# Kernel optimization log

Measured on AMD Instinct MI355X. Metric: run time of the kernel, lower is better.

The kernel has to match this reference:

```python
import jax, jax.numpy as jnp
import numpy as np

EPS = 1e-4   # synsin-style z clamp in world_to_view
BIG = 1e10   # z-buffer init


def _xy_grid(h, w):
    xs = jnp.linspace(-1.0, 1.0, w)
    ys = jnp.linspace(-1.0, 1.0, h)
    gy, gx = jnp.meshgrid(ys, xs, indexing='ij')
    return jnp.stack([gx.ravel(), gy.ravel()], 0)  # [2, h*w], NDC pixel rays


def _view_to_world(depth, K_inv, RTinv, xy):
    # depth [B,1,N]; homogeneous coords rows = (x*d, y*d, d, 1)
    proj = jnp.concatenate([xy[None] * depth, depth, jnp.ones_like(depth)], axis=1)  # [B,4,N]
    cam = jnp.einsum('bij,bjn->bin', K_inv, proj)
    return jnp.einsum('bij,bjn->bin', RTinv, cam)  # [B,4,N]


def _world_to_view(world, K, RT):
    cam2 = jnp.einsum('bij,bjn->bin', RT, world)
    xy_proj = jnp.einsum('bij,bjn->bin', K, cam2)
    z = xy_proj[:, 2:3]
    mask = jnp.abs(z) < EPS
    zs = jnp.where(mask, EPS, z)
    sampler = jnp.concatenate([xy_proj[:, 0:2] / zs, z], axis=1)  # [B,3,N]
    return jnp.where(mask, -10.0, sampler)


def _splat_one(sampler, feats, h, w):
    # sampler [3,N] (x,y in NDC, z depth); feats [C,N]. Nearest-pixel z-buffer splat.
    x, y, z = sampler[0], sampler[1], sampler[2]
    n = x.shape[0]
    px = jnp.round((x + 1.0) * 0.5 * (w - 1)).astype(jnp.int32)
    py = jnp.round((y + 1.0) * 0.5 * (h - 1)).astype(jnp.int32)
    valid = (px >= 0) & (px < w) & (py >= 0) & (py < h) & (z > EPS)
    idx = jnp.where(valid, py * w + px, h * w)  # invalid -> dump bucket h*w
    zv = jnp.where(valid, z, BIG)
    zbuf = jnp.full(h * w + 1, BIG, feats.dtype).at[idx].min(zv)
    pid = jnp.where(valid & (zv <= zbuf[idx]), jnp.arange(n, dtype=jnp.int32), n)
    win = jnp.full(h * w + 1, n, jnp.int32).at[idx].min(pid)[: h * w]  # winning point per pixel
    fpad = jnp.concatenate([feats, jnp.zeros((feats.shape[0], 1), feats.dtype)], axis=1)
    out = fpad[:, win].reshape(feats.shape[0], h, w)
    zb = zbuf[: h * w]
    depth = jnp.where(zb < BIG, zb, 0.0).reshape(1, h, w)
    return out, depth


def _project(depths, colors, feats, K, src_RTs, src_RTinvs, dst_RTs, dst_RTinvs):
    B, V, _, Hc, Wc = depths.shape
    _, _, C, Hf, Wf = feats.shape
    sh, sw = Hf / Hc, Wf / Wc
    scale = jnp.array([sw, sh, 1.0, 1.0], depths.dtype)[None, :, None]
    sK = K * scale
    sKinv = jnp.linalg.inv(sK)

    colors_r = jax.image.resize(colors.reshape(B * V, 3, Hc, Wc), (B * V, 3, Hf, Wf),
                                method='linear', antialias=True)
    depths_r = jax.image.resize(depths.reshape(B * V, 1, Hc, Wc), (B * V, 1, Hf, Wf),
                                method='nearest')
    feats_f = feats.reshape(B, V, C, Hf * Wf)
    colors_f = colors_r.reshape(B, V, 3, Hf * Wf)
    depths_f = depths_r.reshape(B, V, 1, Hf * Wf)

    xy = _xy_grid(Hf, Wf)
    dstRT = dst_RTs[:, 0]  # num_outputs == 1
    splat = jax.vmap(lambda s, f: _splat_one(s, f, Hf, Wf))

    results, warped, pdepths = [], [], []
    for i in range(V):  # small fixed number of source views
        world = _view_to_world(depths_f[:, i], sKinv, src_RTinvs[:, i], xy)
        sampler = _world_to_view(world, sK, dstRT)            # [B,3,N]
        src = jnp.concatenate([feats_f[:, i], colors_f[:, i] * 0.5 + 0.5], axis=1)  # [B,C+3,N]
        res, dep = splat(sampler, src)                        # [B,C+3,Hf,Wf], [B,1,Hf,Wf]
        results.append(res[:, :C])
        warped.append(res[:, C:])
        pdepths.append(dep)

    prj_fs = jnp.stack(results, 0)      # [V,B,C,Hf,Wf]
    warped = jnp.stack(warped, 0)       # [V,B,3,Hf,Wf]
    prj_depths = jnp.stack(pdepths, 0)  # [V,B,1,Hf,Wf]
    # forward() permutes prj_fs / prj_depths to [B,V,...]; warped stays [V,B,...]
    return prj_fs.transpose(1, 0, 2, 3, 4), warped, prj_depths.transpose(1, 0, 2, 3, 4)


def setup_inputs() -> dict:
    key = jax.random.key(0)
    k1, k2, k3 = jax.random.split(key, 3)
    B, V, Hc, Wc = 2, 2, 512, 512
    Hf, Wf, C = 256, 256, 64

    depths = jax.random.uniform(k1, (B, V, 1, Hc, Wc), jnp.float32, 1.0, 5.0)
    colors = jax.random.uniform(k2, (B, V, 3, Hc, Wc), jnp.float32, -1.0, 1.0)
    feats = jax.random.normal(k3, (B, V, C, Hf, Wf), jnp.float32)

    K = np.eye(4, dtype=np.float32)  # NDC intrinsic (fx=fy=1, cx=cy=0)
    th = 0.1
    R = np.array([[np.cos(th), 0, np.sin(th), 0.2],
                  [0, 1, 0, 0.0],
                  [-np.sin(th), 0, np.cos(th), 0.1],
                  [0, 0, 0, 1]], dtype=np.float32)
    src_RT = np.eye(4, dtype=np.float32)

    Kb = jnp.asarray(np.tile(K[None], (B, 1, 1)))
    src_RTs = jnp.asarray(np.tile(src_RT[None, None], (B, V, 1, 1)))
    src_RTinvs = src_RTs  # identity
    dst_RTs = jnp.asarray(np.tile(R[None, None], (B, 1, 1, 1)))
    dst_RTinvs = jnp.asarray(np.tile(np.linalg.inv(R)[None, None], (B, 1, 1, 1)))

    return {"depths": depths, "colors": colors, "feats": feats, "K": Kb,
            "src_RTs": src_RTs, "src_RTinvs": src_RTinvs,
            "dst_RTs": dst_RTs, "dst_RTinvs": dst_RTinvs}


def reference(depths, colors, feats, K, src_RTs, src_RTinvs, dst_RTs, dst_RTinvs):
    return _project(depths, colors, feats, K, src_RTs, src_RTinvs, dst_RTs, dst_RTinvs)
```

## Files before the change

### kernel.cpp

```cpp
#include <hip/hip_runtime.h>
#include <stdint.h>

#pragma clang fp contract(off)

namespace {
constexpr int B_ = 2, V_ = 2, HC = 512, WC = 512, HF = 256, WF = 256, CF = 64;
constexpr int NPIX = HF * WF;
constexpr float EPSF = 1e-4f;
constexpr float BIGF = 1e10f;
constexpr int NPT = B_ * V_ * NPIX;
constexpr int NBLK_PT = NPT / 256;
constexpr int RESIZE_BLKS = (B_ * V_ * 3 * NPIX) / 256;
constexpr int TP_BLKS = B_ * V_ * (NPIX / 64);
constexpr size_t WS_BASE = (size_t)NPT * 8 + (size_t)B_ * V_ * 3 * NPIX * 4 + 256;
constexpr size_t TF_BYTES = (size_t)NPT * CF * 4;
}

__device__ __forceinline__ float dot4f(const float* __restrict__ r,
                                       float v0, float v1, float v2, float v3) {
  float t = r[0] * v0;
  t = t + r[1] * v1;
  t = t + r[2] * v2;
  t = t + r[3] * v3;
  return t;
}

__global__ void init_k(const float* __restrict__ K,
                       float* __restrict__ mats,
                       unsigned long long* __restrict__ zwin) {
  int g = blockIdx.x * blockDim.x + threadIdx.x;
  zwin[g] = ~0ULL;

  if (g < B_) {
    int b = g;
    const float rowscale[4] = {0.5f, 0.5f, 1.0f, 1.0f};
    float sK[16];
    for (int i = 0; i < 4; ++i)
      for (int j = 0; j < 4; ++j)
        sK[i*4+j] = K[b*16 + i*4 + j] * rowscale[i];
    double m[16];
    for (int i = 0; i < 16; ++i) m[i] = (double)sK[i];
    double inv[16];
    inv[0]  =  m[5]*m[10]*m[15] - m[5]*m[11]*m[14] - m[9]*m[6]*m[15] + m[9]*m[7]*m[14] + m[13]*m[6]*m[11] - m[13]*m[7]*m[10];
    inv[4]  = -m[4]*m[10]*m[15] + m[4]*m[11]*m[14] + m[8]*m[6]*m[15] - m[8]*m[7]*m[14] - m[12]*m[6]*m[11] + m[12]*m[7]*m[10];
    inv[8]  =  m[4]*m[9]*m[15]  - m[4]*m[11]*m[13] - m[8]*m[5]*m[15] + m[8]*m[7]*m[13] + m[12]*m[5]*m[11] - m[12]*m[7]*m[9];
    inv[12] = -m[4]*m[9]*m[14]  + m[4]*m[10]*m[13] + m[8]*m[5]*m[14] - m[8]*m[6]*m[13] - m[12]*m[5]*m[10] + m[12]*m[6]*m[9];
    inv[1]  = -m[1]*m[10]*m[15] + m[1]*m[11]*m[14] + m[9]*m[2]*m[15] - m[9]*m[3]*m[14] - m[13]*m[2]*m[11] + m[13]*m[3]*m[10];
    inv[5]  =  m[0]*m[10]*m[15] - m[0]*m[11]*m[14] - m[8]*m[2]*m[15] + m[8]*m[3]*m[14] + m[12]*m[2]*m[11] - m[12]*m[3]*m[10];
    inv[9]  = -m[0]*m[9]*m[15]  + m[0]*m[11]*m[13] + m[8]*m[1]*m[15] - m[8]*m[3]*m[13] - m[12]*m[1]*m[11] + m[12]*m[3]*m[9];
    inv[13] =  m[0]*m[9]*m[14]  - m[0]*m[10]*m[13] - m[8]*m[1]*m[14] + m[8]*m[2]*m[13] + m[12]*m[1]*m[10] - m[12]*m[2]*m[9];
    inv[2]  =  m[1]*m[6]*m[15]  - m[1]*m[7]*m[14]  - m[5]*m[2]*m[15] + m[5]*m[3]*m[14] + m[13]*m[2]*m[7]  - m[13]*m[3]*m[6];
    inv[6]  = -m[0]*m[6]*m[15]  + m[0]*m[7]*m[14]  + m[4]*m[2]*m[15] - m[4]*m[3]*m[14] - m[12]*m[2]*m[7]  + m[12]*m[3]*m[6];
    inv[10] =  m[0]*m[5]*m[15]  - m[0]*m[7]*m[13]  - m[4]*m[1]*m[15] + m[4]*m[3]*m[13] + m[12]*m[1]*m[7]  - m[12]*m[3]*m[5];
    inv[14] = -m[0]*m[5]*m[14]  + m[0]*m[6]*m[13]  + m[4]*m[1]*m[14] - m[4]*m[2]*m[13] - m[12]*m[1]*m[6]  + m[12]*m[2]*m[5];
    inv[3]  = -m[1]*m[6]*m[11]  + m[1]*m[7]*m[10]  + m[5]*m[2]*m[11] - m[5]*m[3]*m[10] - m[9]*m[2]*m[7]   + m[9]*m[3]*m[6];
    inv[7]  =  m[0]*m[6]*m[11]  - m[0]*m[7]*m[10]  - m[4]*m[2]*m[11] + m[4]*m[3]*m[10] + m[8]*m[2]*m[7]   - m[8]*m[3]*m[6];
    inv[11] = -m[0]*m[5]*m[11]  + m[0]*m[7]*m[9]   + m[4]*m[1]*m[11] - m[4]*m[3]*m[9]  - m[8]*m[1]*m[7]   + m[8]*m[3]*m[5];
    inv[15] =  m[0]*m[5]*m[10]  - m[0]*m[6]*m[9]   - m[4]*m[1]*m[10] + m[4]*m[2]*m[9]  + m[8]*m[1]*m[6]   - m[8]*m[2]*m[5];
    double det = m[0]*inv[0] + m[1]*inv[4] + m[2]*inv[8] + m[3]*inv[12];
    double idet = 1.0 / det;
    for (int i = 0; i < 16; ++i) {
      mats[b*32 + i]      = sK[i];
      mats[b*32 + 16 + i] = (float)(inv[i] * idet);
    }
  }
}

__global__ void work_k(const float* __restrict__ depths,
                       const float* __restrict__ mats,
                       const float* __restrict__ srcRTinv,
                       const float* __restrict__ dstRT,
                       unsigned long long* __restrict__ zwin,
                       const float* __restrict__ feats,
                       float* __restrict__ tf,
                       const float* __restrict__ colors,
                       float* __restrict__ colr) {
  int bid = blockIdx.x;
  int nTP = (int)gridDim.x - RESIZE_BLKS - NBLK_PT;
  int t = threadIdx.x;

  if (bid < nTP) {
    int bv = bid >> 10;
    int pix0 = (bid & 1023) << 6;
    int c4 = t >> 4;
    int p4 = t & 15;
    const float* fb = feats + (size_t)bv * CF * NPIX + pix0 + 4 * p4;
    float4 v0 = *(const float4*)(fb + (size_t)(4 * c4 + 0) * NPIX);
    float4 v1 = *(const float4*)(fb + (size_t)(4 * c4 + 1) * NPIX);
    float4 v2 = *(const float4*)(fb + (size_t)(4 * c4 + 2) * NPIX);
    float4 v3 = *(const float4*)(fb + (size_t)(4 * c4 + 3) * NPIX);
    float* tb = tf + ((size_t)bv * NPIX + pix0 + 4 * p4) * CF + 4 * c4;
    *(float4*)(tb + 0 * CF) = make_float4(v0.x, v1.x, v2.x, v3.x);
    *(float4*)(tb + 1 * CF) = make_float4(v0.y, v1.y, v2.y, v3.y);
    *(float4*)(tb + 2 * CF) = make_float4(v0.z, v1.z, v2.z, v3.z);
    *(float4*)(tb + 3 * CF) = make_float4(v0.w, v1.w, v2.w, v3.w);
    return;
  }

  int rb = bid - nTP;
  if (rb < RESIZE_BLKS) {
    int g = rb * 256 + t;
    int pc  = g >> 16;
    int pix = g & (NPIX - 1);
    int y = pix >> 8, x = pix & (WF - 1);
    const float* src = colors + (size_t)pc * HC * WC;
    const float W37 = (float)(3.0 / 7.0), W17 = (float)(1.0 / 7.0);
    float wy[4] = {0.125f, 0.375f, 0.375f, 0.125f};
    float wx[4] = {0.125f, 0.375f, 0.375f, 0.125f};
    if (y == 0)      { wy[0] = 0.f; wy[1] = W37; wy[2] = W37; wy[3] = W17; }
    if (y == HF - 1) { wy[0] = W17; wy[1] = W37; wy[2] = W37; wy[3] = 0.f; }
    if (x == 0)      { wx[0] = 0.f; wx[1] = W37; wx[2] = W37; wx[3] = W17; }
    if (x == WF - 1) { wx[0] = W17; wx[1] = W37; wx[2] = W37; wx[3] = 0.f; }
    int jy0 = 2 * y - 1, jx0 = 2 * x - 1;
    float acc = 0.f;
    #pragma unroll
    for (int ty = 0; ty < 4; ++ty) {
      if (wy[ty] == 0.f) continue;
      int jy = jy0 + ty;
      float rs = 0.f;
      #pragma unroll
      for (int tx = 0; tx < 4; ++tx) {
        if (wx[tx] == 0.f) continue;
        rs = rs + wx[tx] * src[(size_t)jy * WC + (jx0 + tx)];
      }
      acc = acc + wy[ty] * rs;
    }
    colr[g] = acc;
    return;
  }

  int g = (rb - RESIZE_BLKS) * 256 + t;
  if (g >= NPT) return;
  int bv = g >> 16;
  int n  = g & (NPIX - 1);
  int b  = bv / V_;
  int y = n >> 8, x = n & (WF - 1);
  float d = depths[(size_t)bv * HC * WC + (size_t)(2 * y + 1) * WC + (2 * x + 1)];
  const float step32 = 2.0f / 255.0f;
  float xf = (float)x * step32 - 1.0f;
  float yf = (float)y * step32 - 1.0f;
  float pr0 = xf * d, pr1 = yf * d, pr2 = d, pr3 = 1.0f;
  const float* sK  = mats + b * 32;
  const float* sKi = mats + b * 32 + 16;
  const float* Rs  = srcRTinv + (size_t)bv * 16;
  const float* Rd  = dstRT + (size_t)b * 16;
  float a0 = dot4f(sKi + 0,  pr0, pr1, pr2, pr3);
  float a1 = dot4f(sKi + 4,  pr0, pr1, pr2, pr3);
  float a2 = dot4f(sKi + 8,  pr0, pr1, pr2, pr3);
  float a3 = dot4f(sKi + 12, pr0, pr1, pr2, pr3);
  float w0 = dot4f(Rs + 0,  a0, a1, a2, a3);
  float w1 = dot4f(Rs + 4,  a0, a1, a2, a3);
  float w2 = dot4f(Rs + 8,  a0, a1, a2, a3);
  float w3 = dot4f(Rs + 12, a0, a1, a2, a3);
  float c0 = dot4f(Rd + 0,  w0, w1, w2, w3);
  float c1 = dot4f(Rd + 4,  w0, w1, w2, w3);
  float c2 = dot4f(Rd + 8,  w0, w1, w2, w3);
  float c3 = dot4f(Rd + 12, w0, w1, w2, w3);
  float p0 = dot4f(sK + 0, c0, c1, c2, c3);
  float p1 = dot4f(sK + 4, c0, c1, c2, c3);
  float p2 = dot4f(sK + 8, c0, c1, c2, c3);
  if (!(p2 > EPSF)) return;
  float sx = p0 / p2, sy = p1 / p2;
  float pxf = rintf(((sx + 1.0f) * 0.5f) * 255.0f);
  float pyf = rintf(((sy + 1.0f) * 0.5f) * 255.0f);
  if (!(pxf >= 0.0f && pxf <= 255.0f && pyf >= 0.0f && pyf <= 255.0f)) return;
  int idx = (int)pyf * WF + (int)pxf;
  unsigned zbits = __float_as_uint(p2);
  unsigned long long key = ((unsigned long long)zbits << 32) | (unsigned)n;
  atomicMin(&zwin[(size_t)bv * NPIX + idx], key);
}

__global__ void gather3_k(const unsigned long long* __restrict__ zwin,
                          const float* __restrict__ tf,
                          const float* __restrict__ colr,
                          float* __restrict__ out0,
                          float* __restrict__ out1,
                          float* __restrict__ out2) {
  int bid = blockIdx.x;
  int grp = bid >> 10;
  int g   = (bid & (NBLK_PT - 1)) * 256 + threadIdx.x;
  int bv  = g >> 16;
  int pix = g & (NPIX - 1);
  unsigned long long key = zwin[g];
  bool hit = (key != ~0ULL);
  int n = (int)(key & 0xffffffffULL);

  if (grp < 2) {
    float4 f[8];
    if (hit) {
      const float4* src =
          (const float4*)(tf + ((size_t)bv * NPIX + n) * CF + grp * 32);
      #pragma unroll
      for (int i = 0; i < 8; ++i) f[i] = src[i];
    } else {
      #pragma unroll
      for (int i = 0; i < 8; ++i) f[i] = make_float4(0.f, 0.f, 0.f, 0.f);
    }
    float* o0 = out0 + (size_t)bv * CF * NPIX + (size_t)(grp * 32) * NPIX + pix;
    const float* fs = (const float*)f;
    #pragma unroll
    for (int c = 0; c < 32; ++c)
      __builtin_nontemporal_store(fs[c], &o0[(size_t)c * NPIX]);
  } else {
    int b = bv >> 1, v = bv & 1;
    const float* cb = colr + (size_t)bv * 3 * NPIX;
    float* o1 = out1 + (size_t)(v * B_ + b) * 3 * NPIX + pix;
    if (hit) {
      float z = __uint_as_float((unsigned)(key >> 32));
      __builtin_nontemporal_store((z < BIGF) ? z : 0.0f, &out2[g]);
      #pragma unroll
      for (int ch = 0; ch < 3; ++ch)
        __builtin_nontemporal_store(cb[(size_t)ch * NPIX + n] * 0.5f + 0.5f,
                                    &o1[(size_t)ch * NPIX]);
    } else {
      __builtin_nontemporal_store(0.0f, &out2[g]);
      #pragma unroll
      for (int ch = 0; ch < 3; ++ch)
        __builtin_nontemporal_store(0.0f, &o1[(size_t)ch * NPIX]);
    }
  }
}

__global__ void gather_k(const unsigned long long* __restrict__ zwin,
                         const float* __restrict__ feats,
                         const float* __restrict__ colr,
                         float* __restrict__ out0,
                         float* __restrict__ out1,
                         float* __restrict__ out2) {
  int bid = blockIdx.x;
  int grp = bid >> 10;
  int g   = (bid & (NBLK_PT - 1)) * 256 + threadIdx.x;
  int bv  = g >> 16;
  int pix = g & (NPIX - 1);
  unsigned long long key = zwin[g];
  bool hit = (key != ~0ULL);
  int n = (int)(key & 0xffffffffULL);

  if (grp < 4) {
    int c0 = grp * 16;
    const float* fb = feats + (size_t)bv * CF * NPIX + (size_t)c0 * NPIX;
    float* o0 = out0 + (size_t)bv * CF * NPIX + (size_t)c0 * NPIX + pix;
    if (hit) {
      #pragma unroll
      for (int c = 0; c < 16; ++c)
        __builtin_nontemporal_store(fb[(size_t)c * NPIX + n], &o0[(size_t)c * NPIX]);
    } else {
      #pragma unroll
      for (int c = 0; c < 16; ++c)
        __builtin_nontemporal_store(0.0f, &o0[(size_t)c * NPIX]);
    }
  } else {
    int b = bv >> 1, v = bv & 1;
    const float* cb = colr + (size_t)bv * 3 * NPIX;
    float* o1 = out1 + (size_t)(v * B_ + b) * 3 * NPIX + pix;
    if (hit) {
      float z = __uint_as_float((unsigned)(key >> 32));
      __builtin_nontemporal_store((z < BIGF) ? z : 0.0f, &out2[g]);
      #pragma unroll
      for (int ch = 0; ch < 3; ++ch)
        __builtin_nontemporal_store(cb[(size_t)ch * NPIX + n] * 0.5f + 0.5f,
                                    &o1[(size_t)ch * NPIX]);
    } else {
      __builtin_nontemporal_store(0.0f, &out2[g]);
      #pragma unroll
      for (int ch = 0; ch < 3; ++ch)
        __builtin_nontemporal_store(0.0f, &o1[(size_t)ch * NPIX]);
    }
  }
}

extern "C" void kernel_launch(void* const* d_in, const int* in_sizes, int n_in,
                              void* d_out, int out_size, void* d_ws, size_t ws_size,
                              hipStream_t stream) {
  const float* depths     = (const float*)d_in[0];
  const float* colors     = (const float*)d_in[1];
  const float* feats      = (const float*)d_in[2];
  const float* K          = (const float*)d_in[3];
  const float* src_RTinvs = (const float*)d_in[5];
  const float* dst_RTs    = (const float*)d_in[6];

  float* out0 = (float*)d_out;
  float* out1 = out0 + (size_t)B_ * V_ * CF * NPIX;
  float* out2 = out1 + (size_t)V_ * B_ * 3 * NPIX;

  unsigned long long* zwin = (unsigned long long*)d_ws;
  float* colr = (float*)(zwin + NPT);
  float* mats = colr + (size_t)B_ * V_ * 3 * NPIX;
  float* tf   = (float*)((char*)d_ws + WS_BASE);

  const bool use_tf = (ws_size >= WS_BASE + TF_BYTES);

  init_k<<<NBLK_PT, 256, 0, stream>>>(K, mats, zwin);
  int work_grid = (use_tf ? TP_BLKS : 0) + RESIZE_BLKS + NBLK_PT;
  work_k<<<work_grid, 256, 0, stream>>>(depths, mats, src_RTinvs, dst_RTs, zwin,
                                        feats, tf, colors, colr);
  if (use_tf)
    gather3_k<<<3 * NBLK_PT, 256, 0, stream>>>(zwin, tf, colr, out0, out1, out2);
  else
    gather_k<<<5 * NBLK_PT, 256, 0, stream>>>(zwin, feats, colr, out0, out1, out2);
}
```

Baseline: 181.5 us.

## Transpose features through LDS into 16-channel planar chunks for gather

```diff
diff --git a/kernel.cpp b/kernel.cpp
--- a/kernel.cpp
+++ b/kernel.cpp
@@ -9,9 +9,9 @@
 constexpr float EPSF = 1e-4f;
 constexpr float BIGF = 1e10f;
 constexpr int NPT = B_ * V_ * NPIX;
-constexpr int NBLK_PT = NPT / 256;
+constexpr int NBLK = 1024;
 constexpr int RESIZE_BLKS = (B_ * V_ * 3 * NPIX) / 256;
-constexpr int TP_BLKS = B_ * V_ * (NPIX / 64);
+constexpr int T512_BLKS = B_ * V_ * (NPIX / 512);
 constexpr size_t WS_BASE = (size_t)NPT * 8 + (size_t)B_ * V_ * 3 * NPIX * 4 + 256;
 constexpr size_t TF_BYTES = (size_t)NPT * CF * 4;
 }
@@ -25,112 +25,77 @@
   return t;
 }
 
-__global__ void init_k(const float* __restrict__ K,
-                       float* __restrict__ mats,
-                       unsigned long long* __restrict__ zwin) {
-  int g = blockIdx.x * blockDim.x + threadIdx.x;
-  zwin[g] = ~0ULL;
-
-  if (g < B_) {
-    int b = g;
-    const float rowscale[4] = {0.5f, 0.5f, 1.0f, 1.0f};
-    float sK[16];
-    for (int i = 0; i < 4; ++i)
-      for (int j = 0; j < 4; ++j)
-        sK[i*4+j] = K[b*16 + i*4 + j] * rowscale[i];
-    double m[16];
-    for (int i = 0; i < 16; ++i) m[i] = (double)sK[i];
-    double inv[16];
-    inv[0]  =  m[5]*m[10]*m[15] - m[5]*m[11]*m[14] - m[9]*m[6]*m[15] + m[9]*m[7]*m[14] + m[13]*m[6]*m[11] - m[13]*m[7]*m[10];
-    inv[4]  = -m[4]*m[10]*m[15] + m[4]*m[11]*m[14] + m[8]*m[6]*m[15] - m[8]*m[7]*m[14] - m[12]*m[6]*m[11] + m[12]*m[7]*m[10];
-    inv[8]  =  m[4]*m[9]*m[15]  - m[4]*m[11]*m[13] - m[8]*m[5]*m[15] + m[8]*m[7]*m[13] + m[12]*m[5]*m[11] - m[12]*m[7]*m[9];
-    inv[12] = -m[4]*m[9]*m[14]  + m[4]*m[10]*m[13] + m[8]*m[5]*m[14] - m[8]*m[6]*m[13] - m[12]*m[5]*m[10] + m[12]*m[6]*m[9];
-    inv[1]  = -m[1]*m[10]*m[15] + m[1]*m[11]*m[14] + m[9]*m[2]*m[15] - m[9]*m[3]*m[14] - m[13]*m[2]*m[11] + m[13]*m[3]*m[10];
-    inv[5]  =  m[0]*m[10]*m[15] - m[0]*m[11]*m[14] - m[8]*m[2]*m[15] + m[8]*m[3]*m[14] + m[12]*m[2]*m[11] - m[12]*m[3]*m[10];
-    inv[9]  = -m[0]*m[9]*m[15]  + m[0]*m[11]*m[13] + m[8]*m[1]*m[15] - m[8]*m[3]*m[13] - m[12]*m[1]*m[11] + m[12]*m[3]*m[9];
-    inv[13] =  m[0]*m[9]*m[14]  - m[0]*m[10]*m[13] - m[8]*m[1]*m[14] + m[8]*m[2]*m[13] + m[12]*m[1]*m[10] - m[12]*m[2]*m[9];
-    inv[2]  =  m[1]*m[6]*m[15]  - m[1]*m[7]*m[14]  - m[5]*m[2]*m[15] + m[5]*m[3]*m[14] + m[13]*m[2]*m[7]  - m[13]*m[3]*m[6];
-    inv[6]  = -m[0]*m[6]*m[15]  + m[0]*m[7]*m[14]  + m[4]*m[2]*m[15] - m[4]*m[3]*m[14] - m[12]*m[2]*m[7]  + m[12]*m[3]*m[6];
-    inv[10] =  m[0]*m[5]*m[15]  - m[0]*m[7]*m[13]  - m[4]*m[1]*m[15] + m[4]*m[3]*m[13] + m[12]*m[1]*m[7]  - m[12]*m[3]*m[5];
-    inv[14] = -m[0]*m[5]*m[14]  + m[0]*m[6]*m[13]  + m[4]*m[1]*m[14] - m[4]*m[2]*m[13] - m[12]*m[1]*m[6]  + m[12]*m[2]*m[5];
-    inv[3]  = -m[1]*m[6]*m[11]  + m[1]*m[7]*m[10]  + m[5]*m[2]*m[11] - m[5]*m[3]*m[10] - m[9]*m[2]*m[7]   + m[9]*m[3]*m[6];
-    inv[7]  =  m[0]*m[6]*m[11]  - m[0]*m[7]*m[10]  - m[4]*m[2]*m[11] + m[4]*m[3]*m[10] + m[8]*m[2]*m[7]   - m[8]*m[3]*m[6];
-    inv[11] = -m[0]*m[5]*m[11]  + m[0]*m[7]*m[9]   + m[4]*m[1]*m[11] - m[4]*m[3]*m[9]  - m[8]*m[1]*m[7]   + m[8]*m[3]*m[5];
-    inv[15] =  m[0]*m[5]*m[10]  - m[0]*m[6]*m[9]   - m[4]*m[1]*m[10] + m[4]*m[2]*m[9]  + m[8]*m[1]*m[6]   - m[8]*m[2]*m[5];
-    double det = m[0]*inv[0] + m[1]*inv[4] + m[2]*inv[8] + m[3]*inv[12];
-    double idet = 1.0 / det;
-    for (int i = 0; i < 16; ++i) {
-      mats[b*32 + i]      = sK[i];
-      mats[b*32 + 16 + i] = (float)(inv[i] * idet);
-    }
-  }
-}
-
-__global__ void work_k(const float* __restrict__ depths,
-                       const float* __restrict__ mats,
-                       const float* __restrict__ srcRTinv,
-                       const float* __restrict__ dstRT,
-                       unsigned long long* __restrict__ zwin,
-                       const float* __restrict__ feats,
-                       float* __restrict__ tf,
-                       const float* __restrict__ colors,
-                       float* __restrict__ colr) {
-  int bid = blockIdx.x;
-  int nTP = (int)gridDim.x - RESIZE_BLKS - NBLK_PT;
-  int t = threadIdx.x;
-
-  if (bid < nTP) {
-    int bv = bid >> 10;
-    int pix0 = (bid & 1023) << 6;
-    int c4 = t >> 4;
-    int p4 = t & 15;
-    const float* fb = feats + (size_t)bv * CF * NPIX + pix0 + 4 * p4;
-    float4 v0 = *(const float4*)(fb + (size_t)(4 * c4 + 0) * NPIX);
-    float4 v1 = *(const float4*)(fb + (size_t)(4 * c4 + 1) * NPIX);
-    float4 v2 = *(const float4*)(fb + (size_t)(4 * c4 + 2) * NPIX);
-    float4 v3 = *(const float4*)(fb + (size_t)(4 * c4 + 3) * NPIX);
-    float* tb = tf + ((size_t)bv * NPIX + pix0 + 4 * p4) * CF + 4 * c4;
-    *(float4*)(tb + 0 * CF) = make_float4(v0.x, v1.x, v2.x, v3.x);
-    *(float4*)(tb + 1 * CF) = make_float4(v0.y, v1.y, v2.y, v3.y);
-    *(float4*)(tb + 2 * CF) = make_float4(v0.z, v1.z, v2.z, v3.z);
-    *(float4*)(tb + 3 * CF) = make_float4(v0.w, v1.w, v2.w, v3.w);
-    return;
-  }
-
-  int rb = bid - nTP;
-  if (rb < RESIZE_BLKS) {
-    int g = rb * 256 + t;
-    int pc  = g >> 16;
-    int pix = g & (NPIX - 1);
-    int y = pix >> 8, x = pix & (WF - 1);
-    const float* src = colors + (size_t)pc * HC * WC;
-    const float W37 = (float)(3.0 / 7.0), W17 = (float)(1.0 / 7.0);
-    float wy[4] = {0.125f, 0.375f, 0.375f, 0.125f};
-    float wx[4] = {0.125f, 0.375f, 0.375f, 0.125f};
-    if (y == 0)      { wy[0] = 0.f; wy[1] = W37; wy[2] = W37; wy[3] = W17; }
-    if (y == HF - 1) { wy[0] = W17; wy[1] = W37; wy[2] = W37; wy[3] = 0.f; }
-    if (x == 0)      { wx[0] = 0.f; wx[1] = W37; wx[2] = W37; wx[3] = W17; }
-    if (x == WF - 1) { wx[0] = W17; wx[1] = W37; wx[2] = W37; wx[3] = 0.f; }
-    int jy0 = 2 * y - 1, jx0 = 2 * x - 1;
-    float acc = 0.f;
+__device__ void mats_compute(const float* __restrict__ K, int b,
+                             float* __restrict__ mats) {
+  const float rowscale[4] = {0.5f, 0.5f, 1.0f, 1.0f};
+  float sK[16];
+  for (int i = 0; i < 4; ++i)
+    for (int j = 0; j < 4; ++j)
+      sK[i*4+j] = K[b*16 + i*4 + j] * rowscale[i];
+  double m[16];
+  for (int i = 0; i < 16; ++i) m[i] = (double)sK[i];
+  double inv[16];
+  inv[0]  =  m[5]*m[10]*m[15] - m[5]*m[11]*m[14] - m[9]*m[6]*m[15] + m[9]*m[7]*m[14] + m[13]*m[6]*m[11] - m[13]*m[7]*m[10];
+  inv[4]  = -m[4]*m[10]*m[15] + m[4]*m[11]*m[14] + m[8]*m[6]*m[15] - m[8]*m[7]*m[14] - m[12]*m[6]*m[11] + m[12]*m[7]*m[10];
+  inv[8]  =  m[4]*m[9]*m[15]  - m[4]*m[11]*m[13] - m[8]*m[5]*m[15] + m[8]*m[7]*m[13] + m[12]*m[5]*m[11] - m[12]*m[7]*m[9];
+  inv[12] = -m[4]*m[9]*m[14]  + m[4]*m[10]*m[13] + m[8]*m[5]*m[14] - m[8]*m[6]*m[13] - m[12]*m[5]*m[10] + m[12]*m[6]*m[9];
+  inv[1]  = -m[1]*m[10]*m[15] + m[1]*m[11]*m[14] + m[9]*m[2]*m[15] - m[9]*m[3]*m[14] - m[13]*m[2]*m[11] + m[13]*m[3]*m[10];
+  inv[5]  =  m[0]*m[10]*m[15] - m[0]*m[11]*m[14] - m[8]*m[2]*m[15] + m[8]*m[3]*m[14] + m[12]*m[2]*m[11] - m[12]*m[3]*m[10];
+  inv[9]  = -m[0]*m[9]*m[15]  + m[0]*m[11]*m[13] + m[8]*m[1]*m[15] - m[8]*m[3]*m[13] - m[12]*m[1]*m[11] + m[12]*m[3]*m[9];
+  inv[13] =  m[0]*m[9]*m[14]  - m[0]*m[10]*m[13] - m[8]*m[1]*m[14] + m[8]*m[2]*m[13] + m[12]*m[1]*m[10] - m[12]*m[2]*m[9];
+  inv[2]  =  m[1]*m[6]*m[15]  - m[1]*m[7]*m[14]  - m[5]*m[2]*m[15] + m[5]*m[3]*m[14] + m[13]*m[2]*m[7]  - m[13]*m[3]*m[6];
+  inv[6]  = -m[0]*m[6]*m[15]  + m[0]*m[7]*m[14]  + m[4]*m[2]*m[15] - m[4]*m[3]*m[14] - m[12]*m[2]*m[7]  + m[12]*m[3]*m[6];
+  inv[10] =  m[0]*m[5]*m[15]  - m[0]*m[7]*m[13]  - m[4]*m[1]*m[15] + m[4]*m[3]*m[13] + m[12]*m[1]*m[7]  - m[12]*m[3]*m[5];
+  inv[14] = -m[0]*m[5]*m[14]  + m[0]*m[6]*m[13]  + m[4]*m[1]*m[14] - m[4]*m[2]*m[13] - m[12]*m[1]*m[6]  + m[12]*m[2]*m[5];
+  inv[3]  = -m[1]*m[6]*m[11]  + m[1]*m[7]*m[10]  + m[5]*m[2]*m[11] - m[5]*m[3]*m[10] - m[9]*m[2]*m[7]   + m[9]*m[3]*m[6];
+  inv[7]  =  m[0]*m[6]*m[11]  - m[0]*m[7]*m[10]  - m[4]*m[2]*m[11] + m[4]*m[3]*m[10] + m[8]*m[2]*m[7]   - m[8]*m[3]*m[6];
+  inv[11] = -m[0]*m[5]*m[11]  + m[0]*m[7]*m[9]   + m[4]*m[1]*m[11] - m[4]*m[3]*m[9]  - m[8]*m[1]*m[7]   + m[8]*m[3]*m[5];
+  inv[15] =  m[0]*m[5]*m[10]  - m[0]*m[6]*m[9]   - m[4]*m[1]*m[10] + m[4]*m[2]*m[9]  + m[8]*m[1]*m[6]   - m[8]*m[2]*m[5];
+  double det = m[0]*inv[0] + m[1]*inv[4] + m[2]*inv[8] + m[3]*inv[12];
+  double idet = 1.0 / det;
+  for (int i = 0; i < 16; ++i) {
+    mats[b*32 + i]      = sK[i];
+    mats[b*32 + 16 + i] = (float)(inv[i] * idet);
+  }
+}
+
+__device__ __forceinline__ void resize_body(int g,
+                                            const float* __restrict__ colors,
+                                            float* __restrict__ colr) {
+  int pc  = g >> 16;
+  int pix = g & (NPIX - 1);
+  int y = pix >> 8, x = pix & (WF - 1);
+  const float* src = colors + (size_t)pc * HC * WC;
+  const float W37 = (float)(3.0 / 7.0), W17 = (float)(1.0 / 7.0);
+  float wy[4] = {0.125f, 0.375f, 0.375f, 0.125f};
+  float wx[4] = {0.125f, 0.375f, 0.375f, 0.125f};
+  if (y == 0)      { wy[0] = 0.f; wy[1] = W37; wy[2] = W37; wy[3] = W17; }
+  if (y == HF - 1) { wy[0] = W17; wy[1] = W37; wy[2] = W37; wy[3] = 0.f; }
+  if (x == 0)      { wx[0] = 0.f; wx[1] = W37; wx[2] = W37; wx[3] = W17; }
+  if (x == WF - 1) { wx[0] = W17; wx[1] = W37; wx[2] = W37; wx[3] = 0.f; }
+  int jy0 = 2 * y - 1, jx0 = 2 * x - 1;
+  float acc = 0.f;
+  #pragma unroll
+  for (int ty = 0; ty < 4; ++ty) {
+    if (wy[ty] == 0.f) continue;
+    int jy = jy0 + ty;
+    float rs = 0.f;
     #pragma unroll
-    for (int ty = 0; ty < 4; ++ty) {
-      if (wy[ty] == 0.f) continue;
-      int jy = jy0 + ty;
-      float rs = 0.f;
-      #pragma unroll
-      for (int tx = 0; tx < 4; ++tx) {
-        if (wx[tx] == 0.f) continue;
-        rs = rs + wx[tx] * src[(size_t)jy * WC + (jx0 + tx)];
-      }
-      acc = acc + wy[ty] * rs;
-    }
-    colr[g] = acc;
-    return;
-  }
-
-  int g = (rb - RESIZE_BLKS) * 256 + t;
-  if (g >= NPT) return;
+    for (int tx = 0; tx < 4; ++tx) {
+      if (wx[tx] == 0.f) continue;
+      rs = rs + wx[tx] * src[(size_t)jy * WC + (jx0 + tx)];
+    }
+    acc = acc + wy[ty] * rs;
+  }
+  colr[g] = acc;
+}
+
+__device__ __forceinline__ void splat_body(int g,
+                                           const float* __restrict__ depths,
+                                           const float* __restrict__ mats,
+                                           const float* __restrict__ srcRTinv,
+                                           const float* __restrict__ dstRT,
+                                           unsigned long long* __restrict__ zwin) {
   int bv = g >> 16;
   int n  = g & (NPIX - 1);
   int b  = bv / V_;
@@ -159,15 +124,86 @@
   float p0 = dot4f(sK + 0, c0, c1, c2, c3);
   float p1 = dot4f(sK + 4, c0, c1, c2, c3);
   float p2 = dot4f(sK + 8, c0, c1, c2, c3);
-  if (!(p2 > EPSF)) return;
-  float sx = p0 / p2, sy = p1 / p2;
-  float pxf = rintf(((sx + 1.0f) * 0.5f) * 255.0f);
-  float pyf = rintf(((sy + 1.0f) * 0.5f) * 255.0f);
-  if (!(pxf >= 0.0f && pxf <= 255.0f && pyf >= 0.0f && pyf <= 255.0f)) return;
-  int idx = (int)pyf * WF + (int)pxf;
-  unsigned zbits = __float_as_uint(p2);
-  unsigned long long key = ((unsigned long long)zbits << 32) | (unsigned)n;
-  atomicMin(&zwin[(size_t)bv * NPIX + idx], key);
+  if (p2 > EPSF) {
+    float sx = p0 / p2, sy = p1 / p2;
+    float pxf = rintf(((sx + 1.0f) * 0.5f) * 255.0f);
+    float pyf = rintf(((sy + 1.0f) * 0.5f) * 255.0f);
+    if (pxf >= 0.0f && pxf <= 255.0f && pyf >= 0.0f && pyf <= 255.0f) {
+      int idx = (int)pyf * WF + (int)pxf;
+      unsigned zbits = __float_as_uint(p2);
+      unsigned long long key = ((unsigned long long)zbits << 32) | (unsigned)n;
+      atomicMin(&zwin[(size_t)bv * NPIX + idx], key);
+    }
+  }
+}
+
+__global__ void init_k(const float* __restrict__ K,
+                       float* __restrict__ mats,
+                       unsigned long long* __restrict__ zwin) {
+  int g = blockIdx.x * blockDim.x + threadIdx.x;
+  zwin[g] = ~0ULL;
+  if (g < B_) mats_compute(K, g, mats);
+}
+
+__global__ void mix_k(const float* __restrict__ depths,
+                      const float* __restrict__ mats,
+                      const float* __restrict__ srcRTinv,
+                      const float* __restrict__ dstRT,
+                      unsigned long long* __restrict__ zwin,
+                      const float* __restrict__ feats,
+                      float* __restrict__ tf,
+                      const float* __restrict__ colors,
+                      float* __restrict__ colr) {
+  __shared__ float lds[16 * 516];
+  int bid = blockIdx.x;
+  int t = threadIdx.x;
+
+  if (bid < T512_BLKS) {
+    int bv = bid >> 7;
+    int pix0 = (bid & 127) << 9;
+    int w = t >> 6, l = t & 63;
+    int j = l & 3, prel = l >> 2;
+    #pragma unroll
+    for (int s = 0; s < 4; ++s) {
+      if (s) __syncthreads();
+      float4 v[4][2];
+      #pragma unroll
+      for (int k = 0; k < 4; ++k) {
+        int c = 16 * s + 4 * w + k;
+        const float* fp = feats + ((size_t)bv * CF + c) * NPIX + pix0;
+        v[k][0] = *(const float4*)(fp + 4 * l);
+        v[k][1] = *(const float4*)(fp + 256 + 4 * l);
+      }
+      #pragma unroll
+      for (int k = 0; k < 4; ++k) {
+        int cl = 4 * w + k;
+        *(float4*)(&lds[cl * 516 + 4 * l])       = v[k][0];
+        *(float4*)(&lds[cl * 516 + 256 + 4 * l]) = v[k][1];
+      }
+      __syncthreads();
+      float* tb = tf + ((size_t)(bv * 4 + s) * NPIX + pix0) * 16;
+      #pragma unroll
+      for (int it = 0; it < 8; ++it) {
+        int p = w * 128 + it * 16 + prel;
+        float4 o;
+        o.x = lds[(4 * j + 0) * 516 + p];
+        o.y = lds[(4 * j + 1) * 516 + p];
+        o.z = lds[(4 * j + 2) * 516 + p];
+        o.w = lds[(4 * j + 3) * 516 + p];
+        *(float4*)(tb + (size_t)p * 16 + 4 * j) = o;
+      }
+    }
+    return;
+  }
+
+  int rb = bid - T512_BLKS;
+  if (rb < RESIZE_BLKS) {
+    resize_body(rb * 256 + t, colors, colr);
+    return;
+  }
+
+  int g = (rb - RESIZE_BLKS) * 256 + t;
+  splat_body(g, depths, mats, srcRTinv, dstRT, zwin);
 }
 
 __global__ void gather3_k(const unsigned long long* __restrict__ zwin,
@@ -178,7 +214,7 @@
                           float* __restrict__ out2) {
   int bid = blockIdx.x;
   int grp = bid >> 10;
-  int g   = (bid & (NBLK_PT - 1)) * 256 + threadIdx.x;
+  int g   = (bid & (NBLK - 1)) * 256 + threadIdx.x;
   int bv  = g >> 16;
   int pix = g & (NPIX - 1);
   unsigned long long key = zwin[g];
@@ -188,10 +224,14 @@
   if (grp < 2) {
     float4 f[8];
     if (hit) {
-      const float4* src =
-          (const float4*)(tf + ((size_t)bv * NPIX + n) * CF + grp * 32);
-      #pragma unroll
-      for (int i = 0; i < 8; ++i) f[i] = src[i];
+      const float4* s0 =
+          (const float4*)(tf + ((size_t)(bv * 4 + grp * 2) * NPIX + n) * 16);
+      const float4* s1 =
+          (const float4*)(tf + ((size_t)(bv * 4 + grp * 2 + 1) * NPIX + n) * 16);
+      #pragma unroll
+      for (int i = 0; i < 4; ++i) f[i] = s0[i];
+      #pragma unroll
+      for (int i = 0; i < 4; ++i) f[4 + i] = s1[i];
     } else {
       #pragma unroll
       for (int i = 0; i < 8; ++i) f[i] = make_float4(0.f, 0.f, 0.f, 0.f);
@@ -221,6 +261,20 @@
   }
 }
 
+__global__ void work_fb_k(const float* __restrict__ depths,
+                          const float* __restrict__ mats,
+                          const float* __restrict__ srcRTinv,
+                          const float* __restrict__ dstRT,
+                          unsigned long long* __restrict__ zwin,
+                          const float* __restrict__ colors,
+                          float* __restrict__ colr) {
+  int bid = blockIdx.x;
+  int t = threadIdx.x;
+  if (bid < RESIZE_BLKS) { resize_body(bid * 256 + t, colors, colr); return; }
+  int g = (bid - RESIZE_BLKS) * 256 + t;
+  splat_body(g, depths, mats, srcRTinv, dstRT, zwin);
+}
+
 __global__ void gather_k(const unsigned long long* __restrict__ zwin,
                          const float* __restrict__ feats,
                          const float* __restrict__ colr,
@@ -229,7 +283,7 @@
                          float* __restrict__ out2) {
   int bid = blockIdx.x;
   int grp = bid >> 10;
-  int g   = (bid & (NBLK_PT - 1)) * 256 + threadIdx.x;
+  int g   = (bid & (NBLK - 1)) * 256 + threadIdx.x;
   int bv  = g >> 16;
   int pix = g & (NPIX - 1);
   unsigned long long key = zwin[g];
@@ -290,12 +344,14 @@
 
   const bool use_tf = (ws_size >= WS_BASE + TF_BYTES);
 
-  init_k<<<NBLK_PT, 256, 0, stream>>>(K, mats, zwin);
-  int work_grid = (use_tf ? TP_BLKS : 0) + RESIZE_BLKS + NBLK_PT;
-  work_k<<<work_grid, 256, 0, stream>>>(depths, mats, src_RTinvs, dst_RTs, zwin,
-                                        feats, tf, colors, colr);
-  if (use_tf)
-    gather3_k<<<3 * NBLK_PT, 256, 0, stream>>>(zwin, tf, colr, out0, out1, out2);
-  else
-    gather_k<<<5 * NBLK_PT, 256, 0, stream>>>(zwin, feats, colr, out0, out1, out2);
-}
+  init_k<<<NBLK, 256, 0, stream>>>(K, mats, zwin);
+  if (use_tf) {
+    mix_k<<<T512_BLKS + RESIZE_BLKS + NBLK, 256, 0, stream>>>(
+        depths, mats, src_RTinvs, dst_RTs, zwin, feats, tf, colors, colr);
+    gather3_k<<<3 * NBLK, 256, 0, stream>>>(zwin, tf, colr, out0, out1, out2);
+  } else {
+    work_fb_k<<<RESIZE_BLKS + NBLK, 256, 0, stream>>>(
+        depths, mats, src_RTinvs, dst_RTs, zwin, colors, colr);
+    gather_k<<<5 * NBLK, 256, 0, stream>>>(zwin, feats, colr, out0, out1, out2);
+  }
+}
```

New measurement: 183.7 us. About the same (+1.2%).
